# Optimization experiments

Hardware: AMD Instinct MI355X
Metric: run time of the kernel (lower is better)

Reference implementation:

```python
import jax, jax.numpy as jnp
import numpy as np

B, F, E, K, O = 4096, 64, 16, 8, 32
NFEAT, HID = 100000, 1024
EPS = 1e-5
N_ITER = 50  # entmax bisection iterations (entmax package default)


def entmax15(x):
    # alpha=1.5 entmax via bisection, faithful to EntmaxBisectFunction.forward
    d = x.shape[-1]
    xs = x * 0.5  # X * (alpha - 1)
    mx = jnp.max(xs, axis=-1, keepdims=True)
    tau_lo = mx - 1.0                      # gp(1, 1.5) = 1
    tau_hi = mx - (1.0 / d) ** 0.5         # gp(1/d, 1.5)
    f_lo = jnp.sum(jnp.square(jnp.maximum(xs - tau_lo, 0.0)), -1, keepdims=True) - 1.0
    dm = tau_hi - tau_lo

    def body(i, carry):
        tau_lo, dm, _ = carry
        dm = dm * 0.5
        tau_m = tau_lo + dm
        f_m = jnp.sum(jnp.square(jnp.maximum(xs - tau_m, 0.0)), -1, keepdims=True) - 1.0
        tau_lo = jnp.where(f_m * f_lo >= 0, tau_m, tau_lo)
        return (tau_lo, dm, tau_m)

    _, _, tau_m = jax.lax.fori_loop(0, N_ITER, body, (tau_lo, dm, tau_lo))
    p = jnp.square(jnp.maximum(xs - tau_m, 0.0))
    return p / jnp.sum(p, -1, keepdims=True)


def bn_channels(x, g, b):
    # BatchNorm1d on (B, C, L): normalize over batch and L per channel C (train mode)
    m = jnp.mean(x, (0, 2), keepdims=True)
    v = jnp.var(x, (0, 2), keepdims=True)
    return (x - m) / jnp.sqrt(v + EPS) * g[None, :, None] + b[None, :, None]


def bn_feat(x, g, b):
    # BatchNorm1d on (B, C) (train mode, biased variance)
    m = jnp.mean(x, 0)
    v = jnp.var(x, 0)
    return (x - m) / jnp.sqrt(v + EPS) * g + b


def setup_inputs() -> dict:
    key = jax.random.key(0)
    ks = jax.random.split(key, 12)
    gain = 1.414
    aQ = gain * np.sqrt(6.0 / (O + E))
    aB = gain * np.sqrt(6.0 / (E + E))
    aV = gain * np.sqrt(6.0 / (O + F))
    D0 = K * O * E
    return {
        'x_id': jax.random.randint(ks[0], (B, F), 0, NFEAT),
        'x_value': jax.random.uniform(ks[1], (B, F), dtype=jnp.float32),
        'emb': jax.random.normal(ks[2], (NFEAT, E), dtype=jnp.float32) * 0.1,
        'emb_g': jnp.ones((F,), jnp.float32), 'emb_b': jnp.zeros((F,), jnp.float32),
        'Q': jax.random.uniform(ks[3], (K, O, E), jnp.float32, -aQ, aQ),
        'bil': jax.random.uniform(ks[4], (K, E, E), jnp.float32, -aB, aB),
        'vals': jax.random.uniform(ks[5], (K, O, F), jnp.float32, -aV, aV),
        'arm_g': jnp.ones((K * O,), jnp.float32), 'arm_b': jnp.zeros((K * O,), jnp.float32),
        'w1': jax.random.normal(ks[6], (HID, D0), jnp.float32) / np.sqrt(D0),
        'b1': jnp.zeros((HID,), jnp.float32),
        'g1': jnp.ones((HID,), jnp.float32), 'bt1': jnp.zeros((HID,), jnp.float32),
        'w2': jax.random.normal(ks[7], (HID, HID), jnp.float32) / np.sqrt(HID),
        'b2': jnp.zeros((HID,), jnp.float32),
        'g2': jnp.ones((HID,), jnp.float32), 'bt2': jnp.zeros((HID,), jnp.float32),
        'wout': jax.random.normal(ks[8], (1, HID), jnp.float32) / np.sqrt(HID),
        'bout': jnp.zeros((1,), jnp.float32),
    }


def reference(x_id, x_value, emb, emb_g, emb_b, Q, bil, vals, arm_g, arm_b,
              w1, b1, g1, bt1, w2, b2, g2, bt2, wout, bout):
    v = jnp.clip(x_value, 0.001, 1.0)
    xe = emb[x_id] * v[..., None]                       # B,F,E
    x_exp = bn_channels(jnp.exp(xe), emb_g, emb_b)       # B,F,E
    # bilinear attention scores + global context bias
    kq = jnp.einsum('kxy,koy->kox', bil, Q)              # K,O,E (fuse param contraction)
    sc = jnp.einsum('bfx,kox->bkof', xe, kq)             # B,K,O,F
    gc = jnp.einsum('bx,kox->bko', xe.sum(1), kq)        # B,K,O
    sg = entmax15(sc + gc[..., None])                    # B,K,O,F sparse gates
    aw = sg * vals[None]                                 # B,K,O,F
    arm = jnp.einsum('bfe,bkof->bkoe', x_exp, aw)        # B,K,O,E
    arm = arm.reshape(arm.shape[0], K * O, E)
    arm = bn_channels(arm, arm_g, arm_b).reshape(arm.shape[0], -1)
    h = jax.nn.relu(bn_feat(arm @ w1.T + b1, g1, bt1))
    h = jax.nn.relu(bn_feat(h @ w2.T + b2, g2, bt2))
    y = h @ wout.T + bout
    return y[:, 0]
```

## Files before the change

### kernel.cpp

```cpp
#include <hip/hip_runtime.h>

#define EPS 1e-5f

typedef __bf16 bf16;
typedef bf16 bf16x8 __attribute__((ext_vector_type(8)));
typedef float f32x4 __attribute__((ext_vector_type(4)));
typedef float f32x2 __attribute__((ext_vector_type(2)));

__device__ __forceinline__ void lds_cp16(void* lds, const void* g) {
  __builtin_amdgcn_global_load_lds(
      (const __attribute__((address_space(1))) void*)g,
      (__attribute__((address_space(3))) void*)lds, 16, 0, 0);
}

__device__ __forceinline__ f32x4 mfma_bf16(bf16x8 a, bf16x8 b, f32x4 c) {
  return __builtin_amdgcn_mfma_f32_16x16x32_bf16(a, b, c, 0, 0, 0);
}

__global__ void k_embed(const int* __restrict__ x_id, const float* __restrict__ x_val,
                        const float* __restrict__ emb, float* __restrict__ xe,
                        float* __restrict__ es_p, float* __restrict__ eq_p) {
  int t = threadIdx.x, bid = blockIdx.x;
  float s = 0.f, q = 0.f;
#pragma unroll
  for (int it = 0; it < 4; ++it) {
    int g = it * 65536 + bid * 256 + t;
    int id = x_id[g];
    float v = fminf(fmaxf(x_val[g], 0.001f), 1.0f);
    const float4* er = (const float4*)(emb + (size_t)id * 16);
    float4* xo = (float4*)(xe + (size_t)g * 16);
#pragma unroll
    for (int j = 0; j < 4; ++j) {
      float4 e = er[j];
      e.x *= v; e.y *= v; e.z *= v; e.w *= v;
      xo[j] = e;
      float a0 = __expf(e.x), a1 = __expf(e.y), a2 = __expf(e.z), a3 = __expf(e.w);
      s += (a0 + a1) + (a2 + a3);
      q += (a0 * a0 + a1 * a1) + (a2 * a2 + a3 * a3);
    }
  }
  __shared__ float rs[256], rq[256];
  rs[t] = s; rq[t] = q;
  __syncthreads();
  if (t < 64) {
    float S = rs[t] + rs[t + 64] + rs[t + 128] + rs[t + 192];
    float Q = rq[t] + rq[t + 64] + rq[t + 128] + rq[t + 192];
    es_p[bid * 64 + t] = S;
    eq_p[bid * 64 + t] = Q;
  }
}

__global__ void k_prep(const float* __restrict__ Qw, const float* __restrict__ bil,
                       bf16* __restrict__ kqh, bf16* __restrict__ kql,
                       const float* __restrict__ es_p, const float* __restrict__ eq_p,
                       const float* __restrict__ g_, const float* __restrict__ b_,
                       float* __restrict__ oa, float* __restrict__ ob) {
  int t = threadIdx.x;
  int k = t >> 5;
  float qv[16];
#pragma unroll
  for (int y = 0; y < 16; ++y) qv[y] = Qw[t * 16 + y];
  const float* bl = bil + k * 256;
#pragma unroll
  for (int x = 0; x < 16; ++x) {
    float s = 0.f;
#pragma unroll
    for (int y = 0; y < 16; ++y) s += bl[x * 16 + y] * qv[y];
    s *= 0.5f;
    bf16 h = (bf16)s;
    kqh[t * 16 + x] = h;
    kql[t * 16 + x] = (bf16)(s - (float)h);
  }
  if (t < 64) {
    float S = 0.f, Q = 0.f;
    for (int i = 0; i < 256; ++i) { S += es_p[i * 64 + t]; Q += eq_p[i * 64 + t]; }
    float mean = S * (1.0f / 65536.0f);
    float var = Q * (1.0f / 65536.0f) - mean * mean;
    float a = g_[t] * rsqrtf(var + EPS);
    oa[t] = a;
    ob[t] = b_[t] - mean * a;
  }
}

__global__ __launch_bounds__(256, 4) void k_attn(
    const float* __restrict__ xe_g, const bf16* __restrict__ kqh_g,
    const bf16* __restrict__ kql_g, const float* __restrict__ eba,
    const float* __restrict__ ebb, const float* __restrict__ vals,
    bf16* __restrict__ arm) {
  __shared__ __align__(16) unsigned char smem[39168];
  bf16* s_aw = (bf16*)smem;
  float* s_xe = (float*)smem;
  bf16* s_Ah = (bf16*)(smem + 4096);
  bf16* s_Al = (bf16*)(smem + 8192);
  float* s_bn = (float*)(smem + 12288);
  float* s_sum = (float*)(smem + 29696);
  bf16* s_X = (bf16*)(smem + 36864);
  const int t = threadIdx.x;
  const int b = blockIdx.x;
  const int w = t >> 6, lane = t & 63;
  const int q = lane >> 4, ln = lane & 15;
  const f32x4 z4 = {0.f, 0.f, 0.f, 0.f};
  const f32x2 z2 = {0.f, 0.f};

  ((float4*)s_xe)[t] = ((const float4*)(xe_g + (size_t)b * 1024))[t];
  __syncthreads();

  if (t < 16) {
    float s = 0.f;
#pragma unroll
    for (int f = 0; f < 64; ++f) s += s_xe[f * 16 + t];
    s_sum[t] = s;
  }
  {
    int f = t >> 2, e0 = (t & 3) * 4;
    float a = eba[f], c = ebb[f];
#pragma unroll
    for (int j = 0; j < 4; ++j) {
      float v = __expf(s_xe[f * 16 + e0 + j]) * a + c;
      s_X[(e0 + j) * 72 + f] = (bf16)v;
    }
  }
  __syncthreads();

  {
    int f = t >> 2, x0 = (t & 3) * 4;
    union { bf16 h[4]; unsigned long long u; } ph, pl, pz;
    pz.u = 0ull;
#pragma unroll
    for (int j = 0; j < 4; ++j) {
      float v = s_xe[f * 16 + x0 + j] + s_sum[x0 + j];
      bf16 h = (bf16)v;
      ph.h[j] = h;
      pl.h[j] = (bf16)(v - (float)h);
    }
    *(unsigned long long*)(s_Ah + f * 32 + x0) = ph.u;
    *(unsigned long long*)(s_Al + f * 32 + x0) = pl.u;
    *(unsigned long long*)(s_Ah + f * 32 + 16 + x0) = pz.u;
    *(unsigned long long*)(s_Al + f * 32 + 16 + x0) = pz.u;
  }
  __syncthreads();

  bf16x8 Ah[4], Al[4];
#pragma unroll
  for (int ft = 0; ft < 4; ++ft) {
    int row = ft * 16 + ln;
    Ah[ft] = *(const bf16x8*)(s_Ah + row * 32 + q * 8);
    Al[ft] = *(const bf16x8*)(s_Al + row * 32 + q * 8);
  }

  float* bn = s_bn + w * (16 * 68);
  f32x2 xs2[32];
#pragma unroll
  for (int gi = 0; gi < 4; ++gi) {
    const int ko = (w * 4 + gi) * 16 + ln;
    bf16x8 Bh, Bl;
#pragma unroll
    for (int j = 0; j < 8; ++j) { Bh[j] = (bf16)0.f; Bl[j] = (bf16)0.f; }
    if (q < 2) {
      Bh = *(const bf16x8*)(kqh_g + ko * 16 + q * 8);
      Bl = *(const bf16x8*)(kql_g + ko * 16 + q * 8);
    }
#pragma unroll
    for (int ft = 0; ft < 4; ++ft) {
      f32x4 a = z4;
      a = mfma_bf16(Ah[ft], Bh, a);
      a = mfma_bf16(Al[ft], Bh, a);
      a = mfma_bf16(Ah[ft], Bl, a);
      *(f32x4*)(bn + ln * 68 + ft * 16 + q * 4) = a;
    }
    if (q == gi) {
#pragma unroll
      for (int i = 0; i < 16; ++i) {
        f32x4 v = *(const f32x4*)(bn + ln * 68 + i * 4);
        xs2[2 * i] = __builtin_shufflevector(v, v, 0, 1);
        xs2[2 * i + 1] = __builtin_shufflevector(v, v, 2, 3);
      }
    }
  }
  __syncthreads();

  f32x2 m2 = xs2[0];
#pragma unroll
  for (int i = 1; i < 32; ++i) m2 = __builtin_elementwise_max(m2, xs2[i]);
  float mx = fmaxf(m2.x, m2.y);

  float tau_lo = mx - 1.0f;
  float dm = 0.875f;
#pragma unroll
  for (int it = 0; it < 7; ++it) {
    dm *= 0.5f;
    float tm = tau_lo + dm;
    f32x2 t2 = {tm, tm};
    f32x2 c2 = z2;
#pragma unroll
    for (int i = 0; i < 32; ++i) {
      f32x2 d = __builtin_elementwise_max(xs2[i] - t2, z2);
      c2 += d * d;
    }
    tau_lo = ((c2.x + c2.y) - 1.0f >= 0.f) ? tm : tau_lo;
  }
  float tau = tau_lo + dm;
#pragma unroll
  for (int r = 0; r < 2; ++r) {
    f32x2 t2 = {tau, tau};
    f32x2 S2 = z2, Q2 = z2;
    float cnt = 0.f;
#pragma unroll
    for (int i = 0; i < 32; ++i) {
      f32x2 y = xs2[i] - t2;
      f32x2 m = __builtin_elementwise_max(y, z2);
      S2 += m; Q2 += m * m;
      cnt += (y.x > 0.f ? 1.f : 0.f) + (y.y > 0.f ? 1.f : 0.f);
    }
    float S1 = S2.x + S2.y, Q1 = Q2.x + Q2.y;
    float disc = fmaxf(S1 * S1 - cnt * (Q1 - 1.0f), 0.f);
    tau += (S1 - sqrtf(disc)) / cnt;
  }
  f32x2 Zv = z2;
  {
    f32x2 t2 = {tau, tau};
#pragma unroll
    for (int i = 0; i < 32; ++i) {
      f32x2 d = __builtin_elementwise_max(xs2[i] - t2, z2);
      f32x2 p = d * d;
      xs2[i] = p;
      Zv += p;
    }
  }
  float inv = 1.0f / (Zv.x + Zv.y);

  const float4* vg = (const float4*)(vals + t * 64);
#pragma unroll
  for (int f8 = 0; f8 < 64; f8 += 8) {
    float4 v0 = vg[f8 / 4], v1 = vg[f8 / 4 + 1];
    union { bf16 h[8]; uint4 u; } pk;
    pk.h[0] = (bf16)(xs2[f8 / 2].x * inv * v0.x);
    pk.h[1] = (bf16)(xs2[f8 / 2].y * inv * v0.y);
    pk.h[2] = (bf16)(xs2[f8 / 2 + 1].x * inv * v0.z);
    pk.h[3] = (bf16)(xs2[f8 / 2 + 1].y * inv * v0.w);
    pk.h[4] = (bf16)(xs2[f8 / 2 + 2].x * inv * v1.x);
    pk.h[5] = (bf16)(xs2[f8 / 2 + 2].y * inv * v1.y);
    pk.h[6] = (bf16)(xs2[f8 / 2 + 3].x * inv * v1.z);
    pk.h[7] = (bf16)(xs2[f8 / 2 + 3].y * inv * v1.w);
    *(uint4*)(s_aw + t * 72 + f8) = pk.u;
  }
  __syncthreads();

  f32x4 acc[4];
#pragma unroll
  for (int mt = 0; mt < 4; ++mt) acc[mt] = z4;
#pragma unroll
  for (int ks = 0; ks < 2; ++ks) {
    bf16x8 bfrag = *(const bf16x8*)(s_X + ln * 72 + ks * 32 + q * 8);
#pragma unroll
    for (int mt = 0; mt < 4; ++mt) {
      int row = (w * 4 + mt) * 16 + ln;
      bf16x8 afrag = *(const bf16x8*)(s_aw + row * 72 + ks * 32 + q * 8);
      acc[mt] = mfma_bf16(afrag, bfrag, acc[mt]);
    }
  }
  bf16* armb = arm + (size_t)b * 4096;
#pragma unroll
  for (int mt = 0; mt < 4; ++mt) {
    int ko0 = (w * 4 + mt) * 16 + q * 4;
#pragma unroll
    for (int r = 0; r < 4; ++r)
      armb[(ko0 + r) * 16 + ln] = (bf16)acc[mt][r];
  }
}

__global__ void k_armstats(const bf16* __restrict__ arm, float* __restrict__ as_p,
                           float* __restrict__ aq_p) {
  int t = threadIdx.x;
  int b0 = blockIdx.x * 64;
  float s = 0.f, q = 0.f;
  for (int i = 0; i < 64; ++i) {
    const bf16* p = arm + (size_t)(b0 + i) * 4096 + t * 16;
    bf16x8 v0 = *(const bf16x8*)p;
    bf16x8 v1 = *(const bf16x8*)(p + 8);
#pragma unroll
    for (int j = 0; j < 8; ++j) {
      float a = (float)v0[j], c = (float)v1[j];
      s += a + c; q += a * a + c * c;
    }
  }
  as_p[blockIdx.x * 256 + t] = s;
  aq_p[blockIdx.x * 256 + t] = q;
}

__global__ void k_cvtw(const float* __restrict__ w1, const float* __restrict__ w2,
                       const float* __restrict__ as_p, const float* __restrict__ aq_p,
                       const float* __restrict__ arm_g, bf16* __restrict__ d1,
                       bf16* __restrict__ d2) {
  int t = threadIdx.x, bid = blockIdx.x;
  if (bid < 256) {
    __shared__ float scale[256];
    float s = 0.f, q = 0.f;
    for (int i = 0; i < 64; ++i) { s += as_p[i * 256 + t]; q += aq_p[i * 256 + t]; }
    float mean = s * (1.0f / 65536.0f);
    float var = q * (1.0f / 65536.0f) - mean * mean;
    scale[t] = arm_g[t] * rsqrtf(var + EPS);
    __syncthreads();
#pragma unroll
    for (int it = 0; it < 16; ++it) {
      int i = it * 65536 + bid * 256 + t;
      float4 v = ((const float4*)w1)[i];
      float av = scale[(i >> 2) & 255];
      union { bf16 h[4]; uint2 u; } p;
      p.h[0] = (bf16)(v.x * av); p.h[1] = (bf16)(v.y * av);
      p.h[2] = (bf16)(v.z * av); p.h[3] = (bf16)(v.w * av);
      *(uint2*)(d1 + (size_t)i * 4) = p.u;
    }
  } else {
#pragma unroll
    for (int it = 0; it < 16; ++it) {
      int i = it * 16384 + (bid - 256) * 256 + t;
      float4 v = ((const float4*)w2)[i];
      union { bf16 h[4]; uint2 u; } p;
      p.h[0] = (bf16)v.x; p.h[1] = (bf16)v.y; p.h[2] = (bf16)v.z; p.h[3] = (bf16)v.w;
      *(uint2*)(d2 + (size_t)i * 4) = p.u;
    }
  }
}

__global__ __launch_bounds__(256, 2) void gemm_bt(
    const bf16* __restrict__ A, const bf16* __restrict__ Bw, float* __restrict__ C,
    float* __restrict__ sp, float* __restrict__ sq, int Kd) {
  __shared__ __align__(16) bf16 sA[128 * 64];
  __shared__ __align__(16) bf16 sB[64 * 64];
  __shared__ float sredS[4][64], sredQ[4][64];
  const int t = threadIdx.x;
  const int w = t >> 6, lane = t & 63;
  const int m0 = blockIdx.x * 128, n0 = blockIdx.y * 64;

  f32x4 acc[2][4];
#pragma unroll
  for (int i = 0; i < 2; ++i)
#pragma unroll
    for (int j = 0; j < 4; ++j) acc[i][j] = (f32x4){0.f, 0.f, 0.f, 0.f};

  for (int kt = 0; kt < Kd; kt += 64) {
#pragma unroll
    for (int c = 0; c < 4; ++c) {
      int idx = c * 256 + t;
      int row = idx >> 3, ch = idx & 7;
      int sch = ch ^ (row & 7);
      lds_cp16(sA + idx * 8, A + (size_t)(m0 + row) * Kd + kt + sch * 8);
    }
#pragma unroll
    for (int c = 0; c < 2; ++c) {
      int idx = c * 256 + t;
      int row = idx >> 3, ch = idx & 7;
      int sch = ch ^ (row & 7);
      lds_cp16(sB + idx * 8, Bw + (size_t)(n0 + row) * Kd + kt + sch * 8);
    }
    __syncthreads();
#pragma unroll
    for (int ks = 0; ks < 2; ++ks) {
      bf16x8 af[2], bfr[4];
#pragma unroll
      for (int mt = 0; mt < 2; ++mt) {
        int row = w * 32 + mt * 16 + (lane & 15);
        int slot = (ks * 4 + (lane >> 4)) ^ (row & 7);
        af[mt] = *(const bf16x8*)(sA + row * 64 + slot * 8);
      }
#pragma unroll
      for (int nt = 0; nt < 4; ++nt) {
        int row = nt * 16 + (lane & 15);
        int slot = (ks * 4 + (lane >> 4)) ^ (row & 7);
        bfr[nt] = *(const bf16x8*)(sB + row * 64 + slot * 8);
      }
#pragma unroll
      for (int mt = 0; mt < 2; ++mt)
#pragma unroll
        for (int nt = 0; nt < 4; ++nt)
          acc[mt][nt] = mfma_bf16(af[mt], bfr[nt], acc[mt][nt]);
    }
    __syncthreads();
  }

#pragma unroll
  for (int nt = 0; nt < 4; ++nt) {
    int ncol = n0 + nt * 16 + (lane & 15);
    float s = 0.f, q = 0.f;
#pragma unroll
    for (int mt = 0; mt < 2; ++mt) {
      int mr = m0 + w * 32 + mt * 16 + (lane >> 4) * 4;
#pragma unroll
      for (int r = 0; r < 4; ++r) {
        float v = acc[mt][nt][r];
        C[(size_t)(mr + r) * 1024 + ncol] = v;
        s += v; q += v * v;
      }
    }
    s += __shfl_xor(s, 16, 64); s += __shfl_xor(s, 32, 64);
    q += __shfl_xor(q, 16, 64); q += __shfl_xor(q, 32, 64);
    if (lane < 16) { sredS[w][nt * 16 + lane] = s; sredQ[w][nt * 16 + lane] = q; }
  }
  __syncthreads();
  if (t < 64) {
    float S = sredS[0][t] + sredS[1][t] + sredS[2][t] + sredS[3][t];
    float Q = sredQ[0][t] + sredQ[1][t] + sredQ[2][t] + sredQ[3][t];
    sp[blockIdx.x * 1024 + n0 + t] = S;
    sq[blockIdx.x * 1024 + n0 + t] = Q;
  }
}

__global__ void k_colfin(const float* __restrict__ sp, const float* __restrict__ sq,
                         const float* __restrict__ g_, const float* __restrict__ bt,
                         float* __restrict__ a, float* __restrict__ c) {
  int h = blockIdx.x * 256 + threadIdx.x;
  float S = 0.f, Q = 0.f;
  for (int i = 0; i < 32; ++i) { S += sp[i * 1024 + h]; Q += sq[i * 1024 + h]; }
  float mean = S * (1.0f / 4096.0f);
  float var = Q * (1.0f / 4096.0f) - mean * mean;
  float av = g_[h] * rsqrtf(var + EPS);
  a[h] = av;
  c[h] = bt[h] - mean * av;
}

__global__ void k_h1bf(const float* __restrict__ C1, const float* __restrict__ a,
                       const float* __restrict__ c, bf16* __restrict__ H1) {
  int i4 = blockIdx.x * 256 + threadIdx.x;
  int col0 = (i4 * 4) & 1023;
  float4 v = ((const float4*)C1)[i4];
  float4 av = *(const float4*)(a + col0);
  float4 cv = *(const float4*)(c + col0);
  union { bf16 h[4]; uint2 u; } pk;
  pk.h[0] = (bf16)fmaxf(v.x * av.x + cv.x, 0.f);
  pk.h[1] = (bf16)fmaxf(v.y * av.y + cv.y, 0.f);
  pk.h[2] = (bf16)fmaxf(v.z * av.z + cv.z, 0.f);
  pk.h[3] = (bf16)fmaxf(v.w * av.w + cv.w, 0.f);
  *(uint2*)(H1 + (size_t)i4 * 4) = pk.u;
}

__global__ __launch_bounds__(256) void k_out(const float* __restrict__ C2,
                                             const float* __restrict__ a,
                                             const float* __restrict__ c,
                                             const float* __restrict__ wout,
                                             const float* __restrict__ bout,
                                             float* __restrict__ y) {
  int t = threadIdx.x;
  int w = t >> 6, lane = t & 63;
  int row = blockIdx.x * 4 + w;
  const float* cr = C2 + (size_t)row * 1024;
  float s = 0.f;
#pragma unroll
  for (int j = 0; j < 16; ++j) {
    int col = j * 64 + lane;
    float v = fmaxf(cr[col] * a[col] + c[col], 0.f);
    s += v * wout[col];
  }
#pragma unroll
  for (int off = 32; off > 0; off >>= 1) s += __shfl_xor(s, off, 64);
  if (lane == 0) y[row] = s + bout[0];
}

extern "C" void kernel_launch(void* const* d_in, const int* in_sizes, int n_in,
                              void* d_out, int out_size, void* d_ws, size_t ws_size,
                              hipStream_t stream) {
  (void)in_sizes; (void)n_in; (void)out_size; (void)ws_size;
  const int* x_id = (const int*)d_in[0];
  const float* x_value = (const float*)d_in[1];
  const float* emb = (const float*)d_in[2];
  const float* emb_g = (const float*)d_in[3];
  const float* embb = (const float*)d_in[4];
  const float* Qw = (const float*)d_in[5];
  const float* bil = (const float*)d_in[6];
  const float* vals = (const float*)d_in[7];
  const float* arm_g = (const float*)d_in[8];
  const float* w1 = (const float*)d_in[10];
  const float* g1 = (const float*)d_in[12];
  const float* bt1 = (const float*)d_in[13];
  const float* w2 = (const float*)d_in[14];
  const float* g2 = (const float*)d_in[16];
  const float* bt2 = (const float*)d_in[17];
  const float* wout = (const float*)d_in[18];
  const float* bout = (const float*)d_in[19];

  char* w = (char*)d_ws;
  float* ws_A = (float*)w;
  bf16* ws_arm = (bf16*)(w + 16777216);
  bf16* ws_w1b = (bf16*)(w + 50331648);
  bf16* ws_H1 = ws_w1b;
  bf16* ws_w2b = (bf16*)(w + 58720256);
  bf16* ws_kqh = (bf16*)(w + 60817408);
  bf16* ws_kql = (bf16*)(w + 60825600);
  float* misc = (float*)(w + 60833792);
  float* es_p = misc;
  float* eq_p = es_p + 16384;
  float* as_p = eq_p + 16384;
  float* aq_p = as_p + 16384;
  float* sp1 = aq_p + 16384;
  float* sq1 = sp1 + 32768;
  float* sp2 = sq1 + 32768;
  float* sq2 = sp2 + 32768;
  float* eb_a = sq2 + 32768;
  float* eb_b = eb_a + 64;
  float* a1c = eb_b + 64;
  float* c1c = a1c + 1024;
  float* a2c = c1c + 1024;
  float* c2c = a2c + 1024;

  k_embed<<<256, 256, 0, stream>>>(x_id, x_value, emb, ws_A, es_p, eq_p);
  k_prep<<<1, 256, 0, stream>>>(Qw, bil, ws_kqh, ws_kql, es_p, eq_p, emb_g, embb,
                                eb_a, eb_b);
  k_attn<<<4096, 256, 0, stream>>>(ws_A, ws_kqh, ws_kql, eb_a, eb_b, vals, ws_arm);
  k_armstats<<<64, 256, 0, stream>>>(ws_arm, as_p, aq_p);
  k_cvtw<<<320, 256, 0, stream>>>(w1, w2, as_p, aq_p, arm_g, ws_w1b, ws_w2b);
  gemm_bt<<<dim3(32, 16), 256, 0, stream>>>(ws_arm, ws_w1b, ws_A, sp1, sq1, 4096);
  k_colfin<<<4, 256, 0, stream>>>(sp1, sq1, g1, bt1, a1c, c1c);
  k_h1bf<<<4096, 256, 0, stream>>>(ws_A, a1c, c1c, ws_H1);
  gemm_bt<<<dim3(32, 16), 256, 0, stream>>>(ws_H1, ws_w2b, ws_A, sp2, sq2, 1024);
  k_colfin<<<4, 256, 0, stream>>>(sp2, sq2, g2, bt2, a2c, c2c);
  k_out<<<1024, 256, 0, stream>>>(ws_A, a2c, c2c, wout, bout, (float*)d_out);
}
```

Measured before the change: 312.0 us.

## Shrink attention LDS footprint, split arm stats reduction, raise occupancy bounds

The attention kernel now aliases the BN scratch area onto the start of shared memory and builds the weighted gate matrix in two halves of 32 features, which reduces LDS use. Together with a higher launch-bounds block count, this is meant to let more blocks run per CU. The arm-statistics reduction moves from 64 to 512 blocks, and a new single-block finalize kernel computes the scale so the weight-conversion kernel no longer repeats that reduction in every block. The GEMM launch bound also rises to 3. In exchange there are extra barriers, an extra launch, and tighter register budgets that may cause spills.

New measurement: 363.1 us. 1.16x slower.

```diff
diff --git a/kernel.cpp b/kernel.cpp
--- a/kernel.cpp
+++ b/kernel.cpp
@@ -82,19 +82,19 @@
   }
 }
 
-__global__ __launch_bounds__(256, 4) void k_attn(
+__global__ __launch_bounds__(256, 5) void k_attn(
     const float* __restrict__ xe_g, const bf16* __restrict__ kqh_g,
     const bf16* __restrict__ kql_g, const float* __restrict__ eba,
     const float* __restrict__ ebb, const float* __restrict__ vals,
     bf16* __restrict__ arm) {
-  __shared__ __align__(16) unsigned char smem[39168];
+  __shared__ __align__(16) unsigned char smem[22848];
   bf16* s_aw = (bf16*)smem;
   float* s_xe = (float*)smem;
   bf16* s_Ah = (bf16*)(smem + 4096);
   bf16* s_Al = (bf16*)(smem + 8192);
-  float* s_bn = (float*)(smem + 12288);
-  float* s_sum = (float*)(smem + 29696);
-  bf16* s_X = (bf16*)(smem + 36864);
+  float* s_bn = (float*)smem;
+  float* s_sum = (float*)(smem + 20480);
+  bf16* s_X = (bf16*)(smem + 20544);
   const int t = threadIdx.x;
   const int b = blockIdx.x;
   const int w = t >> 6, lane = t & 63;
@@ -147,6 +147,7 @@
     Ah[ft] = *(const bf16x8*)(s_Ah + row * 32 + q * 8);
     Al[ft] = *(const bf16x8*)(s_Al + row * 32 + q * 8);
   }
+  __syncthreads();
 
   float* bn = s_bn + w * (16 * 68);
   f32x2 xs2[32];
@@ -230,34 +231,35 @@
   float inv = 1.0f / (Zv.x + Zv.y);
 
   const float4* vg = (const float4*)(vals + t * 64);
-#pragma unroll
-  for (int f8 = 0; f8 < 64; f8 += 8) {
-    float4 v0 = vg[f8 / 4], v1 = vg[f8 / 4 + 1];
-    union { bf16 h[8]; uint4 u; } pk;
-    pk.h[0] = (bf16)(xs2[f8 / 2].x * inv * v0.x);
-    pk.h[1] = (bf16)(xs2[f8 / 2].y * inv * v0.y);
-    pk.h[2] = (bf16)(xs2[f8 / 2 + 1].x * inv * v0.z);
-    pk.h[3] = (bf16)(xs2[f8 / 2 + 1].y * inv * v0.w);
-    pk.h[4] = (bf16)(xs2[f8 / 2 + 2].x * inv * v1.x);
-    pk.h[5] = (bf16)(xs2[f8 / 2 + 2].y * inv * v1.y);
-    pk.h[6] = (bf16)(xs2[f8 / 2 + 3].x * inv * v1.z);
-    pk.h[7] = (bf16)(xs2[f8 / 2 + 3].y * inv * v1.w);
-    *(uint4*)(s_aw + t * 72 + f8) = pk.u;
-  }
-  __syncthreads();
-
   f32x4 acc[4];
 #pragma unroll
   for (int mt = 0; mt < 4; ++mt) acc[mt] = z4;
 #pragma unroll
-  for (int ks = 0; ks < 2; ++ks) {
-    bf16x8 bfrag = *(const bf16x8*)(s_X + ln * 72 + ks * 32 + q * 8);
+  for (int h = 0; h < 2; ++h) {
+#pragma unroll
+    for (int f8 = 0; f8 < 32; f8 += 8) {
+      int fi = h * 32 + f8;
+      float4 v0 = vg[fi / 4], v1 = vg[fi / 4 + 1];
+      union { bf16 hh[8]; uint4 u; } pk;
+      pk.hh[0] = (bf16)(xs2[fi / 2].x * inv * v0.x);
+      pk.hh[1] = (bf16)(xs2[fi / 2].y * inv * v0.y);
+      pk.hh[2] = (bf16)(xs2[fi / 2 + 1].x * inv * v0.z);
+      pk.hh[3] = (bf16)(xs2[fi / 2 + 1].y * inv * v0.w);
+      pk.hh[4] = (bf16)(xs2[fi / 2 + 2].x * inv * v1.x);
+      pk.hh[5] = (bf16)(xs2[fi / 2 + 2].y * inv * v1.y);
+      pk.hh[6] = (bf16)(xs2[fi / 2 + 3].x * inv * v1.z);
+      pk.hh[7] = (bf16)(xs2[fi / 2 + 3].y * inv * v1.w);
+      *(uint4*)(s_aw + t * 40 + f8) = pk.u;
+    }
+    __syncthreads();
+    bf16x8 bfrag = *(const bf16x8*)(s_X + ln * 72 + h * 32 + q * 8);
 #pragma unroll
     for (int mt = 0; mt < 4; ++mt) {
       int row = (w * 4 + mt) * 16 + ln;
-      bf16x8 afrag = *(const bf16x8*)(s_aw + row * 72 + ks * 32 + q * 8);
+      bf16x8 afrag = *(const bf16x8*)(s_aw + row * 40 + q * 8);
       acc[mt] = mfma_bf16(afrag, bfrag, acc[mt]);
     }
+    if (h == 0) __syncthreads();
   }
   bf16* armb = arm + (size_t)b * 4096;
 #pragma unroll
@@ -272,9 +274,9 @@
 __global__ void k_armstats(const bf16* __restrict__ arm, float* __restrict__ as_p,
                            float* __restrict__ aq_p) {
   int t = threadIdx.x;
-  int b0 = blockIdx.x * 64;
+  int b0 = blockIdx.x * 8;
   float s = 0.f, q = 0.f;
-  for (int i = 0; i < 64; ++i) {
+  for (int i = 0; i < 8; ++i) {
     const bf16* p = arm + (size_t)(b0 + i) * 4096 + t * 16;
     bf16x8 v0 = *(const bf16x8*)p;
     bf16x8 v1 = *(const bf16x8*)(p + 8);
@@ -288,18 +290,23 @@
   aq_p[blockIdx.x * 256 + t] = q;
 }
 
+__global__ void k_armfin(const float* __restrict__ as_p, const float* __restrict__ aq_p,
+                         const float* __restrict__ arm_g, float* __restrict__ scale) {
+  int t = threadIdx.x;
+  float s = 0.f, q = 0.f;
+  for (int i = 0; i < 512; ++i) { s += as_p[i * 256 + t]; q += aq_p[i * 256 + t]; }
+  float mean = s * (1.0f / 65536.0f);
+  float var = q * (1.0f / 65536.0f) - mean * mean;
+  scale[t] = arm_g[t] * rsqrtf(var + EPS);
+}
+
 __global__ void k_cvtw(const float* __restrict__ w1, const float* __restrict__ w2,
-                       const float* __restrict__ as_p, const float* __restrict__ aq_p,
-                       const float* __restrict__ arm_g, bf16* __restrict__ d1,
+                       const float* __restrict__ scale_g, bf16* __restrict__ d1,
                        bf16* __restrict__ d2) {
   int t = threadIdx.x, bid = blockIdx.x;
   if (bid < 256) {
     __shared__ float scale[256];
-    float s = 0.f, q = 0.f;
-    for (int i = 0; i < 64; ++i) { s += as_p[i * 256 + t]; q += aq_p[i * 256 + t]; }
-    float mean = s * (1.0f / 65536.0f);
-    float var = q * (1.0f / 65536.0f) - mean * mean;
-    scale[t] = arm_g[t] * rsqrtf(var + EPS);
+    scale[t] = scale_g[t];
     __syncthreads();
 #pragma unroll
     for (int it = 0; it < 16; ++it) {
@@ -323,7 +330,7 @@
   }
 }
 
-__global__ __launch_bounds__(256, 2) void gemm_bt(
+__global__ __launch_bounds__(256, 3) void gemm_bt(
     const bf16* __restrict__ A, const bf16* __restrict__ Bw, float* __restrict__ C,
     float* __restrict__ sp, float* __restrict__ sq, int Kd) {
   __shared__ __align__(16) bf16 sA[128 * 64];
@@ -490,14 +497,15 @@
   float* es_p = misc;
   float* eq_p = es_p + 16384;
   float* as_p = eq_p + 16384;
-  float* aq_p = as_p + 16384;
-  float* sp1 = aq_p + 16384;
+  float* aq_p = as_p + 131072;
+  float* sp1 = aq_p + 131072;
   float* sq1 = sp1 + 32768;
   float* sp2 = sq1 + 32768;
   float* sq2 = sp2 + 32768;
   float* eb_a = sq2 + 32768;
   float* eb_b = eb_a + 64;
-  float* a1c = eb_b + 64;
+  float* scale = eb_b + 64;
+  float* a1c = scale + 256;
   float* c1c = a1c + 1024;
   float* a2c = c1c + 1024;
   float* c2c = a2c + 1024;
@@ -506,8 +514,9 @@
   k_prep<<<1, 256, 0, stream>>>(Qw, bil, ws_kqh, ws_kql, es_p, eq_p, emb_g, embb,
                                 eb_a, eb_b);
   k_attn<<<4096, 256, 0, stream>>>(ws_A, ws_kqh, ws_kql, eb_a, eb_b, vals, ws_arm);
-  k_armstats<<<64, 256, 0, stream>>>(ws_arm, as_p, aq_p);
-  k_cvtw<<<320, 256, 0, stream>>>(w1, w2, as_p, aq_p, arm_g, ws_w1b, ws_w2b);
+  k_armstats<<<512, 256, 0, stream>>>(ws_arm, as_p, aq_p);
+  k_armfin<<<1, 256, 0, stream>>>(as_p, aq_p, arm_g, scale);
+  k_cvtw<<<320, 256, 0, stream>>>(w1, w2, scale, ws_w1b, ws_w2b);
   gemm_bt<<<dim3(32, 16), 256, 0, stream>>>(ws_arm, ws_w1b, ws_A, sp1, sq1, 4096);
   k_colfin<<<4, 256, 0, stream>>>(sp1, sq1, g1, bt1, a1c, c1c);
   k_h1bf<<<4096, 256, 0, stream>>>(ws_A, a1c, c1c, ws_H1);
```
